# Kernel optimization log

Hardware: AMD Instinct MI355X
Metric: run time of the kernel (lower is better)

Reference implementation:

```python
import jax, jax.numpy as jnp
import numpy as np

INPUT_SIZE = 2048
HIDDEN_SIZE = 2048
BATCH = 4096
COMBINED = INPUT_SIZE + HIDDEN_SIZE


def setup_inputs() -> dict:
    key = jax.random.key(0)
    ks = jax.random.split(key, 11)
    s = 1.0 / np.sqrt(COMBINED)  # torch Linear default init scale
    inp = {
        "x_t": jax.random.normal(ks[0], (BATCH, INPUT_SIZE), jnp.float32),
        "h_prev": jax.random.normal(ks[1], (BATCH, HIDDEN_SIZE), jnp.float32),
        "c_prev": jax.random.normal(ks[2], (BATCH, HIDDEN_SIZE), jnp.float32),
        # torch nn.Linear weights: [out, in]
        "W_f": jax.random.uniform(ks[3], (HIDDEN_SIZE, COMBINED), jnp.float32, -s, s),
        "b_f": jax.random.uniform(ks[4], (HIDDEN_SIZE,), jnp.float32, -s, s),
        "W_i": jax.random.uniform(ks[5], (HIDDEN_SIZE, COMBINED), jnp.float32, -s, s),
        "b_i": jax.random.uniform(ks[6], (HIDDEN_SIZE,), jnp.float32, -s, s),
        "W_c": jax.random.uniform(ks[7], (HIDDEN_SIZE, COMBINED), jnp.float32, -s, s),
        "b_c": jax.random.uniform(ks[8], (HIDDEN_SIZE,), jnp.float32, -s, s),
        "W_o": jax.random.uniform(ks[9], (HIDDEN_SIZE, COMBINED), jnp.float32, -s, s),
        "b_o": jax.random.uniform(ks[10], (HIDDEN_SIZE,), jnp.float32, -s, s),
    }
    return inp


def reference(x_t, h_prev, c_prev, W_f, b_f, W_i, b_i, W_c, b_c, W_o, b_o):
    # combined = cat([h_prev, x_t], dim=1)  -> [B, H + I]
    combined = jnp.concatenate([h_prev, x_t], axis=1)
    # Fuse the four gate GEMMs into one [B, C] x [C, 4H] matmul.
    W = jnp.concatenate([W_f, W_i, W_c, W_o], axis=0)  # [4H, C]
    b = jnp.concatenate([b_f, b_i, b_c, b_o], axis=0)  # [4H]
    gates = combined @ W.T + b  # [B, 4H]
    gf, gi, gc, go = jnp.split(gates, 4, axis=1)
    f_t = jax.nn.sigmoid(gf)
    i_t = jax.nn.sigmoid(gi)
    c_tilde = jnp.tanh(gc)
    o_t = jax.nn.sigmoid(go)
    c_t = f_t * c_prev + i_t * c_tilde
    h_t = o_t * jnp.tanh(c_t)
    return (h_t, c_t)
```

## Files before the change

### kernel.cpp

```cpp
#include <hip/hip_runtime.h>
#include <hip/hip_bf16.h>
#include <cstdint>

#define B_DIM 4096
#define H_DIM 2048
#define I_DIM 2048
#define K_DIM 4096
#define N4    8192

typedef unsigned int u32;
typedef unsigned short u16;
typedef __attribute__((ext_vector_type(4))) float floatx4;
typedef __attribute__((ext_vector_type(8))) short bf16x8;

__device__ static inline u16 f2bf(float f) {
    union { float f; u32 u; } v; v.f = f;
    u32 u = v.u;
    return (u16)((u + 0x7FFFu + ((u >> 16) & 1u)) >> 16);
}
__device__ static inline float bf2f(u16 h) {
    union { u32 u; float f; } v; v.u = ((u32)h) << 16;
    return v.f;
}
__device__ static inline void gload16(const void* g, void* l) {
    __builtin_amdgcn_global_load_lds(
        (const __attribute__((address_space(1))) u32*)g,
        (__attribute__((address_space(3))) u32*)l, 16, 0, 0);
}

__global__ void convert_combined(const float* __restrict__ h_prev,
                                 const float* __restrict__ x_t,
                                 u16* __restrict__ comb) {
    int t = blockIdx.x * blockDim.x + threadIdx.x;
    int base = t * 4;
    int row = base >> 12;
    int col = base & 4095;
    const float* src = (col < H_DIM)
        ? (h_prev + row * H_DIM + col)
        : (x_t    + row * I_DIM + (col - H_DIM));
    float4 v = *(const float4*)src;
    ushort4 o = { f2bf(v.x), f2bf(v.y), f2bf(v.z), f2bf(v.w) };
    *(ushort4*)(comb + base) = o;
}

__global__ void convert_w(const float* __restrict__ Wf, const float* __restrict__ Wi,
                          const float* __restrict__ Wc, const float* __restrict__ Wo,
                          u16* __restrict__ wb) {
    long long t = (long long)blockIdx.x * blockDim.x + threadIdx.x;
    long long base = t * 4;
    int row = (int)(base >> 12);
    int col = (int)(base & 4095);
    int g = row >> 11, j = row & 2047;
    const float* W = (g == 0) ? Wf : (g == 1) ? Wi : (g == 2) ? Wc : Wo;
    float4 v = *(const float4*)(W + (long long)j * K_DIM + col);
    ushort4 o = { f2bf(v.x), f2bf(v.y), f2bf(v.z), f2bf(v.w) };
    *(ushort4*)(wb + base) = o;
}

__global__ __launch_bounds__(256) void gemm_gates(const u16* __restrict__ A,
                                                  const u16* __restrict__ Bm,
                                                  u16* __restrict__ G) {
    __shared__ u16 lsA[128 * 32];
    __shared__ u16 lsB[128 * 32];

    const int tid  = threadIdx.x;
    const int lane = tid & 63;
    const int wave = tid >> 6;
    const int wm   = (wave & 1) * 64;
    const int wn   = (wave >> 1) * 64;
    const int quad = lane >> 4;
    const int r    = lane & 15;
    const int mb   = blockIdx.y * 128;
    const int nb   = blockIdx.x * 128;

    floatx4 acc[4][4];
#pragma unroll
    for (int i = 0; i < 4; i++)
#pragma unroll
        for (int j = 0; j < 4; j++)
            acc[i][j] = (floatx4){0.f, 0.f, 0.f, 0.f};

    for (int kt = 0; kt < K_DIM; kt += 32) {
        __syncthreads();
#pragma unroll
        for (int s = 0; s < 2; s++) {
            int c   = tid + s * 256;
            int row = c >> 2;
            int ko  = (c & 3) * 8;
            gload16(A  + (mb + row) * K_DIM + kt + ko, (char*)lsA + c * 16);
            gload16(Bm + (nb + row) * K_DIM + kt + ko, (char*)lsB + c * 16);
        }
        __syncthreads();

        bf16x8 af[4], bfr[4];
#pragma unroll
        for (int i = 0; i < 4; i++)
            af[i] = *(const bf16x8*)&lsA[(wm + i * 16 + r) * 32 + quad * 8];
#pragma unroll
        for (int j = 0; j < 4; j++)
            bfr[j] = *(const bf16x8*)&lsB[(wn + j * 16 + r) * 32 + quad * 8];
#pragma unroll
        for (int i = 0; i < 4; i++)
#pragma unroll
            for (int j = 0; j < 4; j++)
                acc[i][j] = __builtin_amdgcn_mfma_f32_16x16x32_bf16(
                    af[i], bfr[j], acc[i][j], 0, 0, 0);
    }

#pragma unroll
    for (int i = 0; i < 4; i++)
#pragma unroll
        for (int j = 0; j < 4; j++)
#pragma unroll
            for (int rg = 0; rg < 4; rg++) {
                int grow = mb + wm + i * 16 + quad * 4 + rg;
                int gcol = nb + wn + j * 16 + r;
                G[grow * N4 + gcol] = f2bf(acc[i][j][rg]);
            }
}

__global__ void lstm_epilogue(const u16* __restrict__ G,
                              const float* __restrict__ c_prev,
                              const float* __restrict__ bf_, const float* __restrict__ bi_,
                              const float* __restrict__ bc_, const float* __restrict__ bo_,
                              float* __restrict__ out) {
    int t = blockIdx.x * blockDim.x + threadIdx.x;
    int j = t & 2047;
    int row = t >> 11;
    const u16* g = G + (long long)row * N4 + j;
    float gf = bf2f(g[0])    + bf_[j];
    float gi = bf2f(g[2048]) + bi_[j];
    float gc = bf2f(g[4096]) + bc_[j];
    float go = bf2f(g[6144]) + bo_[j];
    float f  = 1.f / (1.f + __expf(-gf));
    float ii = 1.f / (1.f + __expf(-gi));
    float ct = tanhf(gc);
    float oo = 1.f / (1.f + __expf(-go));
    float c  = f * c_prev[t] + ii * ct;
    float h  = oo * tanhf(c);
    out[t] = h;
    out[B_DIM * H_DIM + t] = c;
}

__global__ void lstm_naive(const float* __restrict__ x_t, const float* __restrict__ h_prev,
                           const float* __restrict__ c_prev,
                           const float* __restrict__ Wf, const float* __restrict__ bf_,
                           const float* __restrict__ Wi, const float* __restrict__ bi_,
                           const float* __restrict__ Wc, const float* __restrict__ bc_,
                           const float* __restrict__ Wo, const float* __restrict__ bo_,
                           float* __restrict__ out) {
    int j = blockIdx.x * blockDim.x + threadIdx.x;
    int b = blockIdx.y;
    const float* hrow = h_prev + (long long)b * H_DIM;
    const float* xrow = x_t   + (long long)b * I_DIM;
    const float* wf = Wf + (long long)j * K_DIM;
    const float* wi = Wi + (long long)j * K_DIM;
    const float* wc = Wc + (long long)j * K_DIM;
    const float* wo = Wo + (long long)j * K_DIM;
    float af = bf_[j], ai = bi_[j], ac = bc_[j], ao = bo_[j];
    for (int k = 0; k < H_DIM; k += 4) {
        float4 v = *(const float4*)(hrow + k);
        float4 a = *(const float4*)(wf + k);
        float4 bqi = *(const float4*)(wi + k);
        float4 cq = *(const float4*)(wc + k);
        float4 dq = *(const float4*)(wo + k);
        af += v.x*a.x + v.y*a.y + v.z*a.z + v.w*a.w;
        ai += v.x*bqi.x + v.y*bqi.y + v.z*bqi.z + v.w*bqi.w;
        ac += v.x*cq.x + v.y*cq.y + v.z*cq.z + v.w*cq.w;
        ao += v.x*dq.x + v.y*dq.y + v.z*dq.z + v.w*dq.w;
    }
    for (int k = 0; k < I_DIM; k += 4) {
        float4 v = *(const float4*)(xrow + k);
        float4 a = *(const float4*)(wf + H_DIM + k);
        float4 bqi = *(const float4*)(wi + H_DIM + k);
        float4 cq = *(const float4*)(wc + H_DIM + k);
        float4 dq = *(const float4*)(wo + H_DIM + k);
        af += v.x*a.x + v.y*a.y + v.z*a.z + v.w*a.w;
        ai += v.x*bqi.x + v.y*bqi.y + v.z*bqi.z + v.w*bqi.w;
        ac += v.x*cq.x + v.y*cq.y + v.z*cq.z + v.w*cq.w;
        ao += v.x*dq.x + v.y*dq.y + v.z*dq.z + v.w*dq.w;
    }
    float f  = 1.f / (1.f + __expf(-af));
    float ii = 1.f / (1.f + __expf(-ai));
    float ct = tanhf(ac);
    float oo = 1.f / (1.f + __expf(-ao));
    int t = b * H_DIM + j;
    float c = f * c_prev[t] + ii * ct;
    out[t] = oo * tanhf(c);
    out[B_DIM * H_DIM + t] = c;
}

extern "C" void kernel_launch(void* const* d_in, const int* in_sizes, int n_in,
                              void* d_out, int out_size, void* d_ws, size_t ws_size,
                              hipStream_t stream) {
    const float* x_t    = (const float*)d_in[0];
    const float* h_prev = (const float*)d_in[1];
    const float* c_prev = (const float*)d_in[2];
    const float* Wf = (const float*)d_in[3];  const float* bf_ = (const float*)d_in[4];
    const float* Wi = (const float*)d_in[5];  const float* bi_ = (const float*)d_in[6];
    const float* Wc = (const float*)d_in[7];  const float* bc_ = (const float*)d_in[8];
    const float* Wo = (const float*)d_in[9];  const float* bo_ = (const float*)d_in[10];
    float* out = (float*)d_out;

    const size_t comb_elems  = (size_t)B_DIM * K_DIM;
    const size_t wb_elems    = (size_t)N4 * K_DIM;
    const size_t gates_elems = (size_t)B_DIM * N4;
    const size_t need = (comb_elems + wb_elems + gates_elems) * sizeof(u16);

    if (ws_size >= need) {
        u16* comb  = (u16*)d_ws;
        u16* wb    = comb + comb_elems;
        u16* gates = wb + wb_elems;
        convert_combined<<<(int)(comb_elems / 4 / 256), 256, 0, stream>>>(h_prev, x_t, comb);
        convert_w<<<(int)(wb_elems / 4 / 256), 256, 0, stream>>>(Wf, Wi, Wc, Wo, wb);
        dim3 grid(N4 / 128, B_DIM / 128);
        gemm_gates<<<grid, 256, 0, stream>>>(comb, wb, gates);
        lstm_epilogue<<<(int)((size_t)B_DIM * H_DIM / 256), 256, 0, stream>>>(
            gates, c_prev, bf_, bi_, bc_, bo_, out);
    } else {
        dim3 grid(H_DIM / 256, B_DIM);
        lstm_naive<<<grid, 256, 0, stream>>>(x_t, h_prev, c_prev,
                                             Wf, bf_, Wi, bi_, Wc, bc_, Wo, bo_, out);
    }
}
```

Before: 592.9 us.

## Fuse LSTM epilogue into GEMM, merge conversions, swizzle LDS tiles

Each GEMM block now loads 32 hidden columns from each of the four gate weight blocks, so every wave holds f/i/c/o for the same hidden index. Bias, activations and the cell update are applied directly from the accumulators. This removes the bf16 gates buffer round-trip and the separate epilogue launch. The two fp32-to-bf16 conversion kernels are merged into one launch with 8-wide vectors, LDS reads use an XOR swizzle to cut bank conflicts, and tanh uses an exp-based approximation, with a small accuracy risk.

```diff
diff --git a/kernel.cpp b/kernel.cpp
--- a/kernel.cpp
+++ b/kernel.cpp
@@ -12,73 +12,85 @@
 typedef unsigned short u16;
 typedef __attribute__((ext_vector_type(4))) float floatx4;
 typedef __attribute__((ext_vector_type(8))) short bf16x8;
+typedef __attribute__((ext_vector_type(8))) unsigned short ushort8_t;
 
 __device__ static inline u16 f2bf(float f) {
     union { float f; u32 u; } v; v.f = f;
     u32 u = v.u;
     return (u16)((u + 0x7FFFu + ((u >> 16) & 1u)) >> 16);
 }
-__device__ static inline float bf2f(u16 h) {
-    union { u32 u; float f; } v; v.u = ((u32)h) << 16;
-    return v.f;
-}
 __device__ static inline void gload16(const void* g, void* l) {
     __builtin_amdgcn_global_load_lds(
         (const __attribute__((address_space(1))) u32*)g,
         (__attribute__((address_space(3))) u32*)l, 16, 0, 0);
 }
-
-__global__ void convert_combined(const float* __restrict__ h_prev,
-                                 const float* __restrict__ x_t,
-                                 u16* __restrict__ comb) {
-    int t = blockIdx.x * blockDim.x + threadIdx.x;
-    int base = t * 4;
-    int row = base >> 12;
-    int col = base & 4095;
-    const float* src = (col < H_DIM)
-        ? (h_prev + row * H_DIM + col)
-        : (x_t    + row * I_DIM + (col - H_DIM));
-    float4 v = *(const float4*)src;
-    ushort4 o = { f2bf(v.x), f2bf(v.y), f2bf(v.z), f2bf(v.w) };
-    *(ushort4*)(comb + base) = o;
-}
-
-__global__ void convert_w(const float* __restrict__ Wf, const float* __restrict__ Wi,
-                          const float* __restrict__ Wc, const float* __restrict__ Wo,
-                          u16* __restrict__ wb) {
-    long long t = (long long)blockIdx.x * blockDim.x + threadIdx.x;
-    long long base = t * 4;
-    int row = (int)(base >> 12);
-    int col = (int)(base & 4095);
-    int g = row >> 11, j = row & 2047;
-    const float* W = (g == 0) ? Wf : (g == 1) ? Wi : (g == 2) ? Wc : Wo;
-    float4 v = *(const float4*)(W + (long long)j * K_DIM + col);
-    ushort4 o = { f2bf(v.x), f2bf(v.y), f2bf(v.z), f2bf(v.w) };
-    *(ushort4*)(wb + base) = o;
-}
-
-__global__ __launch_bounds__(256) void gemm_gates(const u16* __restrict__ A,
-                                                  const u16* __restrict__ Bm,
-                                                  u16* __restrict__ G) {
+__device__ static inline float fast_sig(float x) {
+    return 1.f / (1.f + __expf(-x));
+}
+__device__ static inline float fast_tanh(float x) {
+    float ax = fabsf(x);
+    float t = __expf(-2.f * ax);
+    float r = (1.f - t) / (1.f + t);
+    return copysignf(r, x);
+}
+
+__global__ void convert_all(const float* __restrict__ h_prev, const float* __restrict__ x_t,
+                            const float* __restrict__ Wf, const float* __restrict__ Wi,
+                            const float* __restrict__ Wc, const float* __restrict__ Wo,
+                            u16* __restrict__ comb, u16* __restrict__ wb) {
+    const int bid = blockIdx.x;
+    const float* src;
+    u16* dst;
+    size_t base;
+    if (bid < 8192) {
+        base = ((size_t)bid * 256 + threadIdx.x) * 8;
+        int row = (int)(base >> 12), col = (int)(base & 4095);
+        src = (col < H_DIM) ? h_prev + (size_t)row * H_DIM + col
+                            : x_t    + (size_t)row * I_DIM + (col - H_DIM);
+        dst = comb + base;
+    } else {
+        base = ((size_t)(bid - 8192) * 256 + threadIdx.x) * 8;
+        int row = (int)(base >> 12), col = (int)(base & 4095);
+        int g = row >> 11, jj = row & 2047;
+        const float* W = (g == 0) ? Wf : (g == 1) ? Wi : (g == 2) ? Wc : Wo;
+        src = W + (size_t)jj * K_DIM + col;
+        dst = wb + base;
+    }
+    float4 v0 = *(const float4*)src;
+    float4 v1 = *(const float4*)(src + 4);
+    ushort8_t o = { f2bf(v0.x), f2bf(v0.y), f2bf(v0.z), f2bf(v0.w),
+                    f2bf(v1.x), f2bf(v1.y), f2bf(v1.z), f2bf(v1.w) };
+    *(ushort8_t*)dst = o;
+}
+
+__global__ __launch_bounds__(256) void gemm_lstm(const u16* __restrict__ A,
+                                                 const u16* __restrict__ Bm,
+                                                 const float* __restrict__ c_prev,
+                                                 const float* __restrict__ bf_,
+                                                 const float* __restrict__ bi_,
+                                                 const float* __restrict__ bc_,
+                                                 const float* __restrict__ bo_,
+                                                 float* __restrict__ out) {
     __shared__ u16 lsA[128 * 32];
     __shared__ u16 lsB[128 * 32];
 
-    const int tid  = threadIdx.x;
-    const int lane = tid & 63;
-    const int wave = tid >> 6;
-    const int wm   = (wave & 1) * 64;
-    const int wn   = (wave >> 1) * 64;
-    const int quad = lane >> 4;
-    const int r    = lane & 15;
-    const int mb   = blockIdx.y * 128;
-    const int nb   = blockIdx.x * 128;
+    const int tid   = threadIdx.x;
+    const int lane  = tid & 63;
+    const int wave  = tid >> 6;
+    const int wm    = (wave & 1) * 64;
+    const int wpart = wave >> 1;
+    const int wn    = wpart * 64;
+    const int quad  = lane >> 4;
+    const int r     = lane & 15;
+    const int mb    = blockIdx.y * 128;
+    const int jb    = blockIdx.x * 32;
 
     floatx4 acc[4][4];
 #pragma unroll
     for (int i = 0; i < 4; i++)
 #pragma unroll
-        for (int j = 0; j < 4; j++)
-            acc[i][j] = (floatx4){0.f, 0.f, 0.f, 0.f};
+        for (int g = 0; g < 4; g++)
+            acc[i][g] = (floatx4){0.f, 0.f, 0.f, 0.f};
 
     for (int kt = 0; kt < K_DIM; kt += 32) {
         __syncthreads();
@@ -86,60 +98,53 @@
         for (int s = 0; s < 2; s++) {
             int c   = tid + s * 256;
             int row = c >> 2;
-            int ko  = (c & 3) * 8;
-            gload16(A  + (mb + row) * K_DIM + kt + ko, (char*)lsA + c * 16);
-            gload16(Bm + (nb + row) * K_DIM + kt + ko, (char*)lsB + c * 16);
+            int ko  = ((c & 3) ^ (row & 3)) * 8;
+            gload16(A + (size_t)(mb + row) * K_DIM + kt + ko, (char*)lsA + c * 16);
+            int g    = (row >> 4) & 3;
+            int wrow = g * H_DIM + jb + ((row >> 6) << 4) + (row & 15);
+            gload16(Bm + (size_t)wrow * K_DIM + kt + ko, (char*)lsB + c * 16);
         }
         __syncthreads();
 
+        const int sw = (quad ^ (r & 3)) * 8;
         bf16x8 af[4], bfr[4];
 #pragma unroll
         for (int i = 0; i < 4; i++)
-            af[i] = *(const bf16x8*)&lsA[(wm + i * 16 + r) * 32 + quad * 8];
-#pragma unroll
-        for (int j = 0; j < 4; j++)
-            bfr[j] = *(const bf16x8*)&lsB[(wn + j * 16 + r) * 32 + quad * 8];
+            af[i] = *(const bf16x8*)&lsA[(wm + i * 16 + r) * 32 + sw];
+#pragma unroll
+        for (int g = 0; g < 4; g++)
+            bfr[g] = *(const bf16x8*)&lsB[(wn + g * 16 + r) * 32 + sw];
 #pragma unroll
         for (int i = 0; i < 4; i++)
 #pragma unroll
-            for (int j = 0; j < 4; j++)
-                acc[i][j] = __builtin_amdgcn_mfma_f32_16x16x32_bf16(
-                    af[i], bfr[j], acc[i][j], 0, 0, 0);
-    }
-
-#pragma unroll
-    for (int i = 0; i < 4; i++)
-#pragma unroll
-        for (int j = 0; j < 4; j++)
-#pragma unroll
-            for (int rg = 0; rg < 4; rg++) {
-                int grow = mb + wm + i * 16 + quad * 4 + rg;
-                int gcol = nb + wn + j * 16 + r;
-                G[grow * N4 + gcol] = f2bf(acc[i][j][rg]);
-            }
-}
-
-__global__ void lstm_epilogue(const u16* __restrict__ G,
-                              const float* __restrict__ c_prev,
-                              const float* __restrict__ bf_, const float* __restrict__ bi_,
-                              const float* __restrict__ bc_, const float* __restrict__ bo_,
-                              float* __restrict__ out) {
-    int t = blockIdx.x * blockDim.x + threadIdx.x;
-    int j = t & 2047;
-    int row = t >> 11;
-    const u16* g = G + (long long)row * N4 + j;
-    float gf = bf2f(g[0])    + bf_[j];
-    float gi = bf2f(g[2048]) + bi_[j];
-    float gc = bf2f(g[4096]) + bc_[j];
-    float go = bf2f(g[6144]) + bo_[j];
-    float f  = 1.f / (1.f + __expf(-gf));
-    float ii = 1.f / (1.f + __expf(-gi));
-    float ct = tanhf(gc);
-    float oo = 1.f / (1.f + __expf(-go));
-    float c  = f * c_prev[t] + ii * ct;
-    float h  = oo * tanhf(c);
-    out[t] = h;
-    out[B_DIM * H_DIM + t] = c;
+            for (int g = 0; g < 4; g++)
+                acc[i][g] = __builtin_amdgcn_mfma_f32_16x16x32_bf16(
+                    af[i], bfr[g], acc[i][g], 0, 0, 0);
+    }
+
+    const int j = jb + wpart * 16 + r;
+    const float bfv = bf_[j], biv = bi_[j], bcv = bc_[j], bov = bo_[j];
+#pragma unroll
+    for (int i = 0; i < 4; i++) {
+        int row0 = mb + wm + i * 16 + quad * 4;
+#pragma unroll
+        for (int rg = 0; rg < 4; rg++) {
+            int row = row0 + rg;
+            float gf = acc[i][0][rg] + bfv;
+            float gi = acc[i][1][rg] + biv;
+            float gc = acc[i][2][rg] + bcv;
+            float go = acc[i][3][rg] + bov;
+            float f  = fast_sig(gf);
+            float ii = fast_sig(gi);
+            float ct = fast_tanh(gc);
+            float oo = fast_sig(go);
+            size_t idx = (size_t)row * H_DIM + j;
+            float c = f * c_prev[idx] + ii * ct;
+            float h = oo * fast_tanh(c);
+            out[idx] = h;
+            out[(size_t)B_DIM * H_DIM + idx] = c;
+        }
+    }
 }
 
 __global__ void lstm_naive(const float* __restrict__ x_t, const float* __restrict__ h_prev,
@@ -202,21 +207,16 @@
     const float* Wo = (const float*)d_in[9];  const float* bo_ = (const float*)d_in[10];
     float* out = (float*)d_out;
 
-    const size_t comb_elems  = (size_t)B_DIM * K_DIM;
-    const size_t wb_elems    = (size_t)N4 * K_DIM;
-    const size_t gates_elems = (size_t)B_DIM * N4;
-    const size_t need = (comb_elems + wb_elems + gates_elems) * sizeof(u16);
+    const size_t comb_elems = (size_t)B_DIM * K_DIM;
+    const size_t wb_elems   = (size_t)N4 * K_DIM;
+    const size_t need = (comb_elems + wb_elems) * sizeof(u16);
 
     if (ws_size >= need) {
-        u16* comb  = (u16*)d_ws;
-        u16* wb    = comb + comb_elems;
-        u16* gates = wb + wb_elems;
-        convert_combined<<<(int)(comb_elems / 4 / 256), 256, 0, stream>>>(h_prev, x_t, comb);
-        convert_w<<<(int)(wb_elems / 4 / 256), 256, 0, stream>>>(Wf, Wi, Wc, Wo, wb);
-        dim3 grid(N4 / 128, B_DIM / 128);
-        gemm_gates<<<grid, 256, 0, stream>>>(comb, wb, gates);
-        lstm_epilogue<<<(int)((size_t)B_DIM * H_DIM / 256), 256, 0, stream>>>(
-            gates, c_prev, bf_, bi_, bc_, bo_, out);
+        u16* comb = (u16*)d_ws;
+        u16* wb   = comb + comb_elems;
+        convert_all<<<24576, 256, 0, stream>>>(h_prev, x_t, Wf, Wi, Wc, Wo, comb, wb);
+        dim3 grid(H_DIM / 32, B_DIM / 128);
+        gemm_lstm<<<grid, 256, 0, stream>>>(comb, wb, c_prev, bf_, bi_, bc_, bo_, out);
     } else {
         dim3 grid(H_DIM / 256, B_DIM);
         lstm_naive<<<grid, 256, 0, stream>>>(x_t, h_prev, c_prev,
```

New measurement: 644.9 us. 8.8% more time.
